# Performance work log

Measured on AMD Instinct MI355X. Metric: run time of the kernel, lower is better.

Reference implementation:

```python
import jax, jax.numpy as jnp
import numpy as np

N = 50000; E = 400000; H = 8; D = 32; CD = 768; SD = 128; OUT = 2; HD = H * D


def gat_conv(x, src, dst, W, a_src, a_dst, b):
    """PyG-style GATConv (concat heads, self-loops, LeakyReLU 0.2, eval mode)."""
    n = x.shape[0]
    loops = jnp.arange(n, dtype=src.dtype)
    s = jnp.concatenate([src, loops])
    t = jnp.concatenate([dst, loops])
    h = (x @ W).reshape(n, H, D)                      # [N,H,D]
    a_s = (h * a_src).sum(-1)                          # [N,H]
    a_d = (h * a_dst).sum(-1)                          # [N,H]
    e = jax.nn.leaky_relu(a_s[s] + a_d[t], 0.2)        # [E+N,H]
    m = jax.ops.segment_max(e, t, num_segments=n)
    m = jnp.where(jnp.isfinite(m), m, 0.0)
    ex = jnp.exp(e - m[t])
    den = jax.ops.segment_sum(ex, t, num_segments=n)
    alpha = ex / (den[t] + 1e-16)                      # segment softmax over incoming edges
    out = jax.ops.segment_sum(alpha[:, :, None] * h[s], t, num_segments=n)
    return out.reshape(n, HD) + b


def setup_inputs():
    key = jax.random.key(0)
    ks = jax.random.split(key, 32)
    inp = {}
    inp['content_x'] = jax.random.normal(ks[0], (N, CD), jnp.float32)
    inp['social_x'] = jax.random.normal(ks[1], (N, SD), jnp.float32)
    inp['content_edge_index'] = jax.random.randint(ks[2], (2, E), 0, N, dtype=jnp.int32)
    inp['social_edge_index'] = jax.random.randint(ks[3], (2, E), 0, N, dtype=jnp.int32)
    i = 4
    def mk(shape, scale=0.05):
        nonlocal i
        w = jax.random.normal(ks[i], shape, jnp.float32) * scale
        i += 1
        return w
    # content GAT layers
    inp['Wc0'] = mk((CD, HD)); inp['ac0s'] = mk((H, D)); inp['ac0d'] = mk((H, D)); inp['bc0'] = jnp.zeros((HD,), jnp.float32)
    inp['Wc1'] = mk((HD, HD)); inp['ac1s'] = mk((H, D)); inp['ac1d'] = mk((H, D)); inp['bc1'] = jnp.zeros((HD,), jnp.float32)
    # social GAT layers
    inp['Ws0'] = mk((SD, HD)); inp['as0s'] = mk((H, D)); inp['as0d'] = mk((H, D)); inp['bs0'] = jnp.zeros((HD,), jnp.float32)
    inp['Ws1'] = mk((HD, HD)); inp['as1s'] = mk((H, D)); inp['as1d'] = mk((H, D)); inp['bs1'] = jnp.zeros((HD,), jnp.float32)
    # dual channel attention (Linear(HD,1) each)
    inp['attc_w'] = mk((HD, 1)); inp['attc_b'] = jnp.zeros((1,), jnp.float32)
    inp['atts_w'] = mk((HD, 1)); inp['atts_b'] = jnp.zeros((1,), jnp.float32)
    # MLP head
    inp['fc1_w'] = mk((2 * HD, D)); inp['fc1_b'] = jnp.zeros((D,), jnp.float32)
    inp['fc2_w'] = mk((D, OUT)); inp['fc2_b'] = jnp.zeros((OUT,), jnp.float32)
    return inp


def reference(content_x, social_x, content_edge_index, social_edge_index,
              Wc0, ac0s, ac0d, bc0, Wc1, ac1s, ac1d, bc1,
              Ws0, as0s, as0d, bs0, Ws1, as1s, as1d, bs1,
              attc_w, attc_b, atts_w, atts_b,
              fc1_w, fc1_b, fc2_w, fc2_b):
    cs, cd = content_edge_index[0], content_edge_index[1]
    ss, sd = social_edge_index[0], social_edge_index[1]
    c = jax.nn.elu(gat_conv(content_x, cs, cd, Wc0, ac0s, ac0d, bc0))
    c = jax.nn.elu(gat_conv(c, cs, cd, Wc1, ac1s, ac1d, bc1))
    s = jax.nn.elu(gat_conv(social_x, ss, sd, Ws0, as0s, as0d, bs0))
    s = jax.nn.elu(gat_conv(s, ss, sd, Ws1, as1s, as1d, bs1))
    c_score = jax.nn.sigmoid(c @ attc_w + attc_b)      # [N,1]
    s_score = jax.nn.sigmoid(s @ atts_w + atts_b)      # [N,1]
    w = jax.nn.softmax(jnp.concatenate([c_score, s_score], axis=1), axis=1)  # [N,2]
    x = jnp.concatenate([c * w[:, 0:1], s * w[:, 1:2]], axis=1)
    x = jax.nn.elu(x @ fc1_w + fc1_b)
    x = x @ fc2_w + fc2_b
    return jax.nn.log_softmax(x, axis=1)
```

## Files before the change

### kernel.cpp

```cpp
#include <hip/hip_runtime.h>
#include <cstddef>

#define HD 256
#define NHEAD 8
#define DHEAD 32
#define CAP 64

__global__ __launch_bounds__(256) void zero32_k(int* __restrict__ p, int n) {
    int i = blockIdx.x * 256 + threadIdx.x;
    if (i < n) p[i] = 0;
}

__global__ __launch_bounds__(256) void bucket_fill_k(const int* __restrict__ src,
                                                     const int* __restrict__ dst,
                                                     int* __restrict__ cnt,
                                                     int* __restrict__ bkt, int E) {
    int e = blockIdx.x * 256 + threadIdx.x;
    if (e >= E) return;
    int t = dst[e];
    int pos = atomicAdd(&cnt[t], 1);
    if (pos < CAP) bkt[(size_t)t * CAP + pos] = src[e];
}

__global__ __launch_bounds__(256) void gemm256_k(const float* __restrict__ A,
                                                 const float* __restrict__ B,
                                                 float* __restrict__ C, int M, int K) {
    __shared__ float As[8][132];
    __shared__ float Bs[8][132];
    const int tid = threadIdx.x;
    const int bm = blockIdx.y * 128;
    const int bn = blockIdx.x * 128;
    const int ty = tid >> 4, tx = tid & 15;

    const int arow = tid >> 1, akc = (tid & 1) * 4;
    int grow = bm + arow; if (grow > M - 1) grow = M - 1;
    const float* aptr = A + (size_t)grow * K + akc;

    const int bkr = tid >> 5, bcol = (tid & 31) * 4;
    const float* bptr = B + (size_t)bkr * HD + bn + bcol;

    float acc[8][8];
#pragma unroll
    for (int i = 0; i < 8; i++)
#pragma unroll
        for (int j = 0; j < 8; j++) acc[i][j] = 0.f;

    for (int k0 = 0; k0 < K; k0 += 8) {
        float4 av = *(const float4*)aptr; aptr += 8;
        float4 bv = *(const float4*)bptr; bptr += 8 * HD;
        __syncthreads();
        As[akc + 0][arow] = av.x;
        As[akc + 1][arow] = av.y;
        As[akc + 2][arow] = av.z;
        As[akc + 3][arow] = av.w;
        *(float4*)&Bs[bkr][bcol] = bv;
        __syncthreads();
#pragma unroll
        for (int kk = 0; kk < 8; kk++) {
            float af[8], bf[8];
            *(float4*)(af)     = *(const float4*)&As[kk][ty * 8];
            *(float4*)(af + 4) = *(const float4*)&As[kk][ty * 8 + 4];
            *(float4*)(bf)     = *(const float4*)&Bs[kk][tx * 8];
            *(float4*)(bf + 4) = *(const float4*)&Bs[kk][tx * 8 + 4];
#pragma unroll
            for (int i = 0; i < 8; i++)
#pragma unroll
                for (int j = 0; j < 8; j++)
                    acc[i][j] = fmaf(af[i], bf[j], acc[i][j]);
        }
    }
#pragma unroll
    for (int i = 0; i < 8; i++) {
        int r = bm + ty * 8 + i;
        if (r < M) {
            float* cp = C + (size_t)r * HD + bn + tx * 8;
            *(float4*)cp       = make_float4(acc[i][0], acc[i][1], acc[i][2], acc[i][3]);
            *(float4*)(cp + 4) = make_float4(acc[i][4], acc[i][5], acc[i][6], acc[i][7]);
        }
    }
}

__global__ __launch_bounds__(256) void attscore_k(const float* __restrict__ h,
                                                  const float* __restrict__ a_src,
                                                  const float* __restrict__ a_dst,
                                                  float* __restrict__ out_s,
                                                  float* __restrict__ out_d, int n) {
    int idx = blockIdx.x * 256 + threadIdx.x;
    if (idx >= n * NHEAD) return;
    int head = idx & 7;
    const float* hp = h + (size_t)(idx >> 3) * HD + head * DHEAD;
    const float* ap = a_src + head * DHEAD;
    const float* dp = a_dst + head * DHEAD;
    float s = 0.f, d = 0.f;
#pragma unroll
    for (int j = 0; j < DHEAD; j += 4) {
        float4 hv = *(const float4*)(hp + j);
        float4 av = *(const float4*)(ap + j);
        float4 dv = *(const float4*)(dp + j);
        s += hv.x * av.x + hv.y * av.y + hv.z * av.z + hv.w * av.w;
        d += hv.x * dv.x + hv.y * dv.y + hv.z * dv.z + hv.w * dv.w;
    }
    out_s[idx] = s;
    out_d[idx] = d;
}

__device__ __forceinline__ float leaky02(float x) { return x > 0.f ? x : 0.2f * x; }

__global__ __launch_bounds__(256) void agg_k(const float* __restrict__ h,
                                             const float* __restrict__ a_s,
                                             const float* __restrict__ a_d,
                                             const int* __restrict__ cnt,
                                             const int* __restrict__ bkt,
                                             const float* __restrict__ bias,
                                             float* __restrict__ out, int n) {
    int wid = (blockIdx.x * 256 + threadIdx.x) >> 6;
    if (wid >= n) return;
    int lane = threadIdx.x & 63;
    int head = lane >> 3;
    const float4* h4 = (const float4*)h;

    float adt = a_d[wid * NHEAD + head];
    float m = leaky02(a_s[wid * NHEAD + head] + adt);
    float den = 1.f;
    float4 hv = h4[(size_t)wid * 64 + lane];
    float ax = hv.x, ay = hv.y, az = hv.z, aw = hv.w;

    int k = cnt[wid]; if (k > CAP) k = CAP;
    const int* bp = bkt + (size_t)wid * CAP;
    for (int i = 0; i < k; i++) {
        int s = bp[i];
        float e = leaky02(a_s[s * NHEAD + head] + adt);
        float nm = fmaxf(m, e);
        float corr = __expf(m - nm);
        float p = __expf(e - nm);
        float4 v = h4[(size_t)s * 64 + lane];
        den = den * corr + p;
        ax = ax * corr + p * v.x;
        ay = ay * corr + p * v.y;
        az = az * corr + p * v.z;
        aw = aw * corr + p * v.w;
        m = nm;
    }
    float inv = 1.f / den;
    float4 bv = *(const float4*)(bias + lane * 4);
    float ox = fmaf(ax, inv, bv.x);
    float oy = fmaf(ay, inv, bv.y);
    float oz = fmaf(az, inv, bv.z);
    float ow = fmaf(aw, inv, bv.w);
    ox = ox > 0.f ? ox : expm1f(ox);
    oy = oy > 0.f ? oy : expm1f(oy);
    oz = oz > 0.f ? oz : expm1f(oz);
    ow = ow > 0.f ? ow : expm1f(ow);
    ((float4*)out)[(size_t)wid * 64 + lane] = make_float4(ox, oy, oz, ow);
}

__global__ __launch_bounds__(256) void head_k(const float* __restrict__ cb,
                                              const float* __restrict__ sb,
                                              const float* __restrict__ attc_w,
                                              const float* __restrict__ attc_b,
                                              const float* __restrict__ atts_w,
                                              const float* __restrict__ atts_b,
                                              const float* __restrict__ fc1_w,
                                              const float* __restrict__ fc1_b,
                                              const float* __restrict__ fc2_w,
                                              const float* __restrict__ fc2_b,
                                              float* __restrict__ out, int n) {
    int wid = (blockIdx.x * 256 + threadIdx.x) >> 6;
    if (wid >= n) return;
    int lane = threadIdx.x & 63;
    const float* c = cb + (size_t)wid * HD;
    const float* s = sb + (size_t)wid * HD;

    float4 cv = *(const float4*)(c + lane * 4);
    float4 wc = *(const float4*)(attc_w + lane * 4);
    float4 sv = *(const float4*)(s + lane * 4);
    float4 ws = *(const float4*)(atts_w + lane * 4);
    float pc = cv.x * wc.x + cv.y * wc.y + cv.z * wc.z + cv.w * wc.w;
    float ps = sv.x * ws.x + sv.y * ws.y + sv.z * ws.z + sv.w * ws.w;
#pragma unroll
    for (int o = 32; o; o >>= 1) { pc += __shfl_xor(pc, o); ps += __shfl_xor(ps, o); }
    float csc = 1.f / (1.f + __expf(-(pc + attc_b[0])));
    float ssc = 1.f / (1.f + __expf(-(ps + atts_b[0])));
    float mx0 = fmaxf(csc, ssc);
    float e0 = __expf(csc - mx0), e1 = __expf(ssc - mx0);
    float w0 = e0 / (e0 + e1), w1 = e1 / (e0 + e1);

    int col = lane & 31, half = lane >> 5;
    const float* xb = half ? s : c;
    float wsc = half ? w1 : w0;
    const float* fw = fc1_w + (size_t)half * HD * 32 + col;
    float acc = 0.f;
#pragma unroll 4
    for (int kk = 0; kk < HD; kk++) acc = fmaf(xb[kk], fw[kk * 32], acc);
    acc *= wsc;
    float y = acc + __shfl_xor(acc, 32) + fc1_b[col];
    y = y > 0.f ? y : expm1f(y);
    float v = y * fc2_w[col * 2 + half];
#pragma unroll
    for (int o = 16; o; o >>= 1) v += __shfl_xor(v, o);
    float z0 = __shfl(v, 0), z1 = __shfl(v, 32);
    if (lane == 0) {
        float zm = fmaxf(z0, z1);
        float lse = zm + log1pf(__expf(fminf(z0, z1) - zm));
        out[(size_t)wid * 2]     = z0 - lse;
        out[(size_t)wid * 2 + 1] = z1 - lse;
    }
}

extern "C" void kernel_launch(void* const* d_in, const int* in_sizes, int n_in,
                              void* d_out, int out_size, void* d_ws, size_t ws_size,
                              hipStream_t stream) {
    (void)n_in; (void)out_size; (void)ws_size;
    const float* content_x = (const float*)d_in[0];
    const float* social_x  = (const float*)d_in[1];
    const int*   cei = (const int*)d_in[2];
    const int*   sei = (const int*)d_in[3];
    const float* Wc0  = (const float*)d_in[4];
    const float* ac0s = (const float*)d_in[5];
    const float* ac0d = (const float*)d_in[6];
    const float* bc0  = (const float*)d_in[7];
    const float* Wc1  = (const float*)d_in[8];
    const float* ac1s = (const float*)d_in[9];
    const float* ac1d = (const float*)d_in[10];
    const float* bc1  = (const float*)d_in[11];
    const float* Ws0  = (const float*)d_in[12];
    const float* as0s = (const float*)d_in[13];
    const float* as0d = (const float*)d_in[14];
    const float* bs0  = (const float*)d_in[15];
    const float* Ws1  = (const float*)d_in[16];
    const float* as1s = (const float*)d_in[17];
    const float* as1d = (const float*)d_in[18];
    const float* bs1  = (const float*)d_in[19];
    const float* attc_w = (const float*)d_in[20];
    const float* attc_b = (const float*)d_in[21];
    const float* atts_w = (const float*)d_in[22];
    const float* atts_b = (const float*)d_in[23];
    const float* fc1_w  = (const float*)d_in[24];
    const float* fc1_b  = (const float*)d_in[25];
    const float* fc2_w  = (const float*)d_in[26];
    const float* fc2_b  = (const float*)d_in[27];

    const int E  = in_sizes[2] / 2;
    const int CD = in_sizes[4] / HD;
    const int SD = in_sizes[12] / HD;
    const int n  = in_sizes[0] / CD;

    char* p = (char*)d_ws;
    auto carve = [&](size_t bytes) { char* q = p; p += (bytes + 255) & ~(size_t)255; return q; };
    float* hbuf = (float*)carve((size_t)n * HD * 4);
    float* cbuf = (float*)carve((size_t)n * HD * 4);
    float* sbuf = (float*)carve((size_t)n * HD * 4);
    float* asb  = (float*)carve((size_t)n * NHEAD * 4);
    float* adb  = (float*)carve((size_t)n * NHEAD * 4);
    int* cnt_c  = (int*)carve((size_t)n * 4);
    int* cnt_s  = (int*)carve((size_t)n * 4);
    int* bkt_c  = (int*)carve((size_t)n * CAP * 4);
    int* bkt_s  = (int*)carve((size_t)n * CAP * 4);

    zero32_k<<<dim3((n + 255) / 256), 256, 0, stream>>>(cnt_c, n);
    zero32_k<<<dim3((n + 255) / 256), 256, 0, stream>>>(cnt_s, n);
    bucket_fill_k<<<dim3((E + 255) / 256), 256, 0, stream>>>(cei, cei + E, cnt_c, bkt_c, E);
    bucket_fill_k<<<dim3((E + 255) / 256), 256, 0, stream>>>(sei, sei + E, cnt_s, bkt_s, E);

    dim3 gg(2, (n + 127) / 128);
    dim3 nb8((n * NHEAD + 255) / 256);
    dim3 nwave((n + 3) / 4);

    gemm256_k<<<gg, 256, 0, stream>>>(content_x, Wc0, hbuf, n, CD);
    attscore_k<<<nb8, 256, 0, stream>>>(hbuf, ac0s, ac0d, asb, adb, n);
    agg_k<<<nwave, 256, 0, stream>>>(hbuf, asb, adb, cnt_c, bkt_c, bc0, cbuf, n);
    gemm256_k<<<gg, 256, 0, stream>>>(cbuf, Wc1, hbuf, n, HD);
    attscore_k<<<nb8, 256, 0, stream>>>(hbuf, ac1s, ac1d, asb, adb, n);
    agg_k<<<nwave, 256, 0, stream>>>(hbuf, asb, adb, cnt_c, bkt_c, bc1, cbuf, n);
    gemm256_k<<<gg, 256, 0, stream>>>(social_x, Ws0, hbuf, n, SD);
    attscore_k<<<nb8, 256, 0, stream>>>(hbuf, as0s, as0d, asb, adb, n);
    agg_k<<<nwave, 256, 0, stream>>>(hbuf, asb, adb, cnt_s, bkt_s, bs0, sbuf, n);
    gemm256_k<<<gg, 256, 0, stream>>>(sbuf, Ws1, hbuf, n, HD);
    attscore_k<<<nb8, 256, 0, stream>>>(hbuf, as1s, as1d, asb, adb, n);
    agg_k<<<nwave, 256, 0, stream>>>(hbuf, asb, adb, cnt_s, bkt_s, bs1, sbuf, n);

    head_k<<<nwave, 256, 0, stream>>>(cbuf, sbuf, attc_w, attc_b, atts_w, atts_b,
                                      fc1_w, fc1_b, fc2_w, fc2_b, (float*)d_out, n);
}
```

Baseline: 1.397 ms.

## Replace FP32 SIMT GEMM with split-bf16 MFMA GEMM using direct-to-LDS loads

Replaces the scalar FP32 GEMM with a matrix-core kernel that emulates FP32 through a three-term bf16 hi/lo split (hi*hi + hi*lo + lo*hi). Inputs and weights are pre-split into bf16 hi/lo buffers. The layer-0 aggregation kernel writes its output already split, which feeds the layer-1 GEMM. Tiles are staged through swizzled LDS with global_load_lds. The intent is to move the dominant GEMM cost (especially the 768-wide content projection) onto MFMA units. The cost is extra split passes, added memory traffic, and a small loss of accuracy from dropping the lo*lo term.

```diff
diff --git a/kernel.cpp b/kernel.cpp
--- a/kernel.cpp
+++ b/kernel.cpp
@@ -1,10 +1,28 @@
 #include <hip/hip_runtime.h>
 #include <cstddef>
+#include <cstdint>
 
 #define HD 256
 #define NHEAD 8
-#define DHEAD 32
 #define CAP 64
+
+typedef __attribute__((ext_vector_type(8))) short bf16x8;
+typedef __attribute__((ext_vector_type(4))) float f32x4;
+
+__device__ __forceinline__ unsigned short f2bf(float f) {
+    unsigned u = __float_as_uint(f);
+    u += 0x7fffu + ((u >> 16) & 1u);
+    return (unsigned short)(u >> 16);
+}
+__device__ __forceinline__ float bf2f(unsigned short h) {
+    return __uint_as_float(((unsigned)h) << 16);
+}
+
+__device__ __forceinline__ void gload16(const unsigned short* g, unsigned short* l) {
+    __builtin_amdgcn_global_load_lds((const __attribute__((address_space(1))) unsigned int*)g,
+                                     (__attribute__((address_space(3))) unsigned int*)l,
+                                     16, 0, 0);
+}
 
 __global__ __launch_bounds__(256) void zero32_k(int* __restrict__ p, int n) {
     int i = blockIdx.x * 256 + threadIdx.x;
@@ -22,60 +40,123 @@
     if (pos < CAP) bkt[(size_t)t * CAP + pos] = src[e];
 }
 
-__global__ __launch_bounds__(256) void gemm256_k(const float* __restrict__ A,
-                                                 const float* __restrict__ B,
-                                                 float* __restrict__ C, int M, int K) {
-    __shared__ float As[8][132];
-    __shared__ float Bs[8][132];
+__global__ __launch_bounds__(256) void split_k(const float* __restrict__ x,
+                                               unsigned short* __restrict__ hi,
+                                               unsigned short* __restrict__ lo,
+                                               int n4) {
+    int i = blockIdx.x * 256 + threadIdx.x;
+    int stride = gridDim.x * 256;
+    for (; i < n4; i += stride) {
+        float4 v = ((const float4*)x)[i];
+        ushort4 h, l;
+        h.x = f2bf(v.x); l.x = f2bf(v.x - bf2f(h.x));
+        h.y = f2bf(v.y); l.y = f2bf(v.y - bf2f(h.y));
+        h.z = f2bf(v.z); l.z = f2bf(v.z - bf2f(h.z));
+        h.w = f2bf(v.w); l.w = f2bf(v.w - bf2f(h.w));
+        ((ushort4*)hi)[i] = h;
+        ((ushort4*)lo)[i] = l;
+    }
+}
+
+__global__ __launch_bounds__(256) void wsplit_k(const float* __restrict__ W,
+                                                unsigned short* __restrict__ hi,
+                                                unsigned short* __restrict__ lo, int K) {
+    int idx = blockIdx.x * 256 + threadIdx.x;
+    if (idx >= K * HD) return;
+    int n = idx / K, k = idx - n * K;
+    float v = W[(size_t)k * HD + n];
+    unsigned short h = f2bf(v);
+    hi[idx] = h;
+    lo[idx] = f2bf(v - bf2f(h));
+}
+
+__global__ __launch_bounds__(256, 2) void gemm_mfma_k(
+    const unsigned short* __restrict__ Ahi, const unsigned short* __restrict__ Alo,
+    const unsigned short* __restrict__ Bhi, const unsigned short* __restrict__ Blo,
+    float* __restrict__ C, int M, int K) {
+    __shared__ unsigned short smem[4 * 128 * 32];
     const int tid = threadIdx.x;
+    const int lane = tid & 63;
+    const int wv = tid >> 6;
+    const int Rw = (wv >> 1) * 64;
+    const int Cw = (wv & 1) * 64;
     const int bm = blockIdx.y * 128;
     const int bn = blockIdx.x * 128;
-    const int ty = tid >> 4, tx = tid & 15;
-
-    const int arow = tid >> 1, akc = (tid & 1) * 4;
-    int grow = bm + arow; if (grow > M - 1) grow = M - 1;
-    const float* aptr = A + (size_t)grow * K + akc;
-
-    const int bkr = tid >> 5, bcol = (tid & 31) * 4;
-    const float* bptr = B + (size_t)bkr * HD + bn + bcol;
-
-    float acc[8][8];
-#pragma unroll
-    for (int i = 0; i < 8; i++)
-#pragma unroll
-        for (int j = 0; j < 8; j++) acc[i][j] = 0.f;
-
-    for (int k0 = 0; k0 < K; k0 += 8) {
-        float4 av = *(const float4*)aptr; aptr += 8;
-        float4 bv = *(const float4*)bptr; bptr += 8 * HD;
+
+    const int sr0 = tid >> 2;
+    const int p = tid & 3;
+    const int g0 = p ^ ((sr0 >> 1) & 3);
+    const int g1 = p ^ (((sr0 + 64) >> 1) & 3);
+    int ar0 = bm + sr0;      if (ar0 >= M) ar0 = M - 1;
+    int ar1 = bm + sr0 + 64; if (ar1 >= M) ar1 = M - 1;
+    const int bc0 = bn + sr0;
+    const int bc1 = bn + sr0 + 64;
+    const size_t aoff0 = (size_t)ar0 * K + g0 * 8;
+    const size_t aoff1 = (size_t)ar1 * K + g1 * 8;
+    const size_t boff0 = (size_t)bc0 * K + g0 * 8;
+    const size_t boff1 = (size_t)bc1 * K + g1 * 8;
+
+    unsigned short* sAh = smem;
+    unsigned short* sAl = smem + 4096;
+    unsigned short* sBh = smem + 8192;
+    unsigned short* sBl = smem + 12288;
+    const int ldsb = wv * 512;
+
+    f32x4 acc[4][4];
+#pragma unroll
+    for (int m = 0; m < 4; m++)
+#pragma unroll
+        for (int n = 0; n < 4; n++) acc[m][n] = (f32x4){0.f, 0.f, 0.f, 0.f};
+
+    const int r16 = lane & 15, gq = lane >> 4;
+    const int rsw = gq ^ ((r16 >> 1) & 3);
+
+    for (int k0 = 0; k0 < K; k0 += 32) {
         __syncthreads();
-        As[akc + 0][arow] = av.x;
-        As[akc + 1][arow] = av.y;
-        As[akc + 2][arow] = av.z;
-        As[akc + 3][arow] = av.w;
-        *(float4*)&Bs[bkr][bcol] = bv;
+        gload16(Ahi + aoff0 + k0, sAh + ldsb);
+        gload16(Ahi + aoff1 + k0, sAh + 2048 + ldsb);
+        gload16(Alo + aoff0 + k0, sAl + ldsb);
+        gload16(Alo + aoff1 + k0, sAl + 2048 + ldsb);
+        gload16(Bhi + boff0 + k0, sBh + ldsb);
+        gload16(Bhi + boff1 + k0, sBh + 2048 + ldsb);
+        gload16(Blo + boff0 + k0, sBl + ldsb);
+        gload16(Blo + boff1 + k0, sBl + 2048 + ldsb);
         __syncthreads();
-#pragma unroll
-        for (int kk = 0; kk < 8; kk++) {
-            float af[8], bf[8];
-            *(float4*)(af)     = *(const float4*)&As[kk][ty * 8];
-            *(float4*)(af + 4) = *(const float4*)&As[kk][ty * 8 + 4];
-            *(float4*)(bf)     = *(const float4*)&Bs[kk][tx * 8];
-            *(float4*)(bf + 4) = *(const float4*)&Bs[kk][tx * 8 + 4];
-#pragma unroll
-            for (int i = 0; i < 8; i++)
-#pragma unroll
-                for (int j = 0; j < 8; j++)
-                    acc[i][j] = fmaf(af[i], bf[j], acc[i][j]);
+
+        bf16x8 ah[4], al[4], bh[4], bl[4];
+#pragma unroll
+        for (int m = 0; m < 4; m++) {
+            int off = (Rw + m * 16 + r16) * 32 + rsw * 8;
+            ah[m] = *(const bf16x8*)(sAh + off);
+            al[m] = *(const bf16x8*)(sAl + off);
         }
-    }
-#pragma unroll
-    for (int i = 0; i < 8; i++) {
-        int r = bm + ty * 8 + i;
-        if (r < M) {
-            float* cp = C + (size_t)r * HD + bn + tx * 8;
-            *(float4*)cp       = make_float4(acc[i][0], acc[i][1], acc[i][2], acc[i][3]);
-            *(float4*)(cp + 4) = make_float4(acc[i][4], acc[i][5], acc[i][6], acc[i][7]);
+#pragma unroll
+        for (int n = 0; n < 4; n++) {
+            int off = (Cw + n * 16 + r16) * 32 + rsw * 8;
+            bh[n] = *(const bf16x8*)(sBh + off);
+            bl[n] = *(const bf16x8*)(sBl + off);
+        }
+#pragma unroll
+        for (int m = 0; m < 4; m++)
+#pragma unroll
+            for (int n = 0; n < 4; n++) {
+                acc[m][n] = __builtin_amdgcn_mfma_f32_16x16x32_bf16(ah[m], bh[n], acc[m][n], 0, 0, 0);
+                acc[m][n] = __builtin_amdgcn_mfma_f32_16x16x32_bf16(ah[m], bl[n], acc[m][n], 0, 0, 0);
+                acc[m][n] = __builtin_amdgcn_mfma_f32_16x16x32_bf16(al[m], bh[n], acc[m][n], 0, 0, 0);
+            }
+    }
+
+#pragma unroll
+    for (int m = 0; m < 4; m++) {
+        int rbase = bm + Rw + m * 16 + ((lane >> 4) << 2);
+#pragma unroll
+        for (int n = 0; n < 4; n++) {
+            int col = bn + Cw + n * 16 + r16;
+            float* cp = C + (size_t)rbase * HD + col;
+            f32x4 v = acc[m][n];
+#pragma unroll
+            for (int r = 0; r < 4; r++)
+                if (rbase + r < M) cp[(size_t)r * HD] = v[r];
         }
     }
 }
@@ -88,12 +169,12 @@
     int idx = blockIdx.x * 256 + threadIdx.x;
     if (idx >= n * NHEAD) return;
     int head = idx & 7;
-    const float* hp = h + (size_t)(idx >> 3) * HD + head * DHEAD;
-    const float* ap = a_src + head * DHEAD;
-    const float* dp = a_dst + head * DHEAD;
+    const float* hp = h + (size_t)(idx >> 3) * HD + head * 32;
+    const float* ap = a_src + head * 32;
+    const float* dp = a_dst + head * 32;
     float s = 0.f, d = 0.f;
 #pragma unroll
-    for (int j = 0; j < DHEAD; j += 4) {
+    for (int j = 0; j < 32; j += 4) {
         float4 hv = *(const float4*)(hp + j);
         float4 av = *(const float4*)(ap + j);
         float4 dv = *(const float4*)(dp + j);
@@ -112,7 +193,9 @@
                                              const int* __restrict__ cnt,
                                              const int* __restrict__ bkt,
                                              const float* __restrict__ bias,
-                                             float* __restrict__ out, int n) {
+                                             float* __restrict__ out,
+                                             unsigned short* __restrict__ ohi,
+                                             unsigned short* __restrict__ olo, int n) {
     int wid = (blockIdx.x * 256 + threadIdx.x) >> 6;
     if (wid >= n) return;
     int lane = threadIdx.x & 63;
@@ -132,13 +215,13 @@
         float e = leaky02(a_s[s * NHEAD + head] + adt);
         float nm = fmaxf(m, e);
         float corr = __expf(m - nm);
-        float p = __expf(e - nm);
+        float pp = __expf(e - nm);
         float4 v = h4[(size_t)s * 64 + lane];
-        den = den * corr + p;
-        ax = ax * corr + p * v.x;
-        ay = ay * corr + p * v.y;
-        az = az * corr + p * v.z;
-        aw = aw * corr + p * v.w;
+        den = den * corr + pp;
+        ax = ax * corr + pp * v.x;
+        ay = ay * corr + pp * v.y;
+        az = az * corr + pp * v.z;
+        aw = aw * corr + pp * v.w;
         m = nm;
     }
     float inv = 1.f / den;
@@ -152,6 +235,15 @@
     oz = oz > 0.f ? oz : expm1f(oz);
     ow = ow > 0.f ? ow : expm1f(ow);
     ((float4*)out)[(size_t)wid * 64 + lane] = make_float4(ox, oy, oz, ow);
+    if (ohi) {
+        ushort4 h4o, l4o;
+        h4o.x = f2bf(ox); l4o.x = f2bf(ox - bf2f(h4o.x));
+        h4o.y = f2bf(oy); l4o.y = f2bf(oy - bf2f(h4o.y));
+        h4o.z = f2bf(oz); l4o.z = f2bf(oz - bf2f(h4o.z));
+        h4o.w = f2bf(ow); l4o.w = f2bf(ow - bf2f(h4o.w));
+        ((ushort4*)ohi)[(size_t)wid * 64 + lane] = h4o;
+        ((ushort4*)olo)[(size_t)wid * 64 + lane] = l4o;
+    }
 }
 
 __global__ __launch_bounds__(256) void head_k(const float* __restrict__ cb,
@@ -250,35 +342,55 @@
     float* hbuf = (float*)carve((size_t)n * HD * 4);
     float* cbuf = (float*)carve((size_t)n * HD * 4);
     float* sbuf = (float*)carve((size_t)n * HD * 4);
+    unsigned short* Xhi = (unsigned short*)carve((size_t)n * CD * 2);
+    unsigned short* Xlo = (unsigned short*)carve((size_t)n * CD * 2);
     float* asb  = (float*)carve((size_t)n * NHEAD * 4);
     float* adb  = (float*)carve((size_t)n * NHEAD * 4);
     int* cnt_c  = (int*)carve((size_t)n * 4);
     int* cnt_s  = (int*)carve((size_t)n * 4);
     int* bkt_c  = (int*)carve((size_t)n * CAP * 4);
     int* bkt_s  = (int*)carve((size_t)n * CAP * 4);
-
-    zero32_k<<<dim3((n + 255) / 256), 256, 0, stream>>>(cnt_c, n);
-    zero32_k<<<dim3((n + 255) / 256), 256, 0, stream>>>(cnt_s, n);
-    bucket_fill_k<<<dim3((E + 255) / 256), 256, 0, stream>>>(cei, cei + E, cnt_c, bkt_c, E);
-    bucket_fill_k<<<dim3((E + 255) / 256), 256, 0, stream>>>(sei, sei + E, cnt_s, bkt_s, E);
+    unsigned short* Wc0h = (unsigned short*)carve((size_t)CD * HD * 2);
+    unsigned short* Wc0l = (unsigned short*)carve((size_t)CD * HD * 2);
+    unsigned short* Wc1h = (unsigned short*)carve((size_t)HD * HD * 2);
+    unsigned short* Wc1l = (unsigned short*)carve((size_t)HD * HD * 2);
+    unsigned short* Ws0h = (unsigned short*)carve((size_t)SD * HD * 2);
+    unsigned short* Ws0l = (unsigned short*)carve((size_t)SD * HD * 2);
+    unsigned short* Ws1h = (unsigned short*)carve((size_t)HD * HD * 2);
+    unsigned short* Ws1l = (unsigned short*)carve((size_t)HD * HD * 2);
+
+    dim3 b256(256);
+    zero32_k<<<dim3((n + 255) / 256), b256, 0, stream>>>(cnt_c, n);
+    zero32_k<<<dim3((n + 255) / 256), b256, 0, stream>>>(cnt_s, n);
+    bucket_fill_k<<<dim3((E + 255) / 256), b256, 0, stream>>>(cei, cei + E, cnt_c, bkt_c, E);
+    bucket_fill_k<<<dim3((E + 255) / 256), b256, 0, stream>>>(sei, sei + E, cnt_s, bkt_s, E);
+
+    wsplit_k<<<dim3((CD * HD + 255) / 256), b256, 0, stream>>>(Wc0, Wc0h, Wc0l, CD);
+    wsplit_k<<<dim3((HD * HD + 255) / 256), b256, 0, stream>>>(Wc1, Wc1h, Wc1l, HD);
+    wsplit_k<<<dim3((SD * HD + 255) / 256), b256, 0, stream>>>(Ws0, Ws0h, Ws0l, SD);
+    wsplit_k<<<dim3((HD * HD + 255) / 256), b256, 0, stream>>>(Ws1, Ws1h, Ws1l, HD);
 
     dim3 gg(2, (n + 127) / 128);
     dim3 nb8((n * NHEAD + 255) / 256);
     dim3 nwave((n + 3) / 4);
 
-    gemm256_k<<<gg, 256, 0, stream>>>(content_x, Wc0, hbuf, n, CD);
-    attscore_k<<<nb8, 256, 0, stream>>>(hbuf, ac0s, ac0d, asb, adb, n);
-    agg_k<<<nwave, 256, 0, stream>>>(hbuf, asb, adb, cnt_c, bkt_c, bc0, cbuf, n);
-    gemm256_k<<<gg, 256, 0, stream>>>(cbuf, Wc1, hbuf, n, HD);
-    attscore_k<<<nb8, 256, 0, stream>>>(hbuf, ac1s, ac1d, asb, adb, n);
-    agg_k<<<nwave, 256, 0, stream>>>(hbuf, asb, adb, cnt_c, bkt_c, bc1, cbuf, n);
-    gemm256_k<<<gg, 256, 0, stream>>>(social_x, Ws0, hbuf, n, SD);
-    attscore_k<<<nb8, 256, 0, stream>>>(hbuf, as0s, as0d, asb, adb, n);
-    agg_k<<<nwave, 256, 0, stream>>>(hbuf, asb, adb, cnt_s, bkt_s, bs0, sbuf, n);
-    gemm256_k<<<gg, 256, 0, stream>>>(sbuf, Ws1, hbuf, n, HD);
-    attscore_k<<<nb8, 256, 0, stream>>>(hbuf, as1s, as1d, asb, adb, n);
-    agg_k<<<nwave, 256, 0, stream>>>(hbuf, asb, adb, cnt_s, bkt_s, bs1, sbuf, n);
-
-    head_k<<<nwave, 256, 0, stream>>>(cbuf, sbuf, attc_w, attc_b, atts_w, atts_b,
-                                      fc1_w, fc1_b, fc2_w, fc2_b, (float*)d_out, n);
-}
+    split_k<<<dim3(2048), b256, 0, stream>>>(content_x, Xhi, Xlo, n * CD / 4);
+    gemm_mfma_k<<<gg, b256, 0, stream>>>(Xhi, Xlo, Wc0h, Wc0l, hbuf, n, CD);
+    attscore_k<<<nb8, b256, 0, stream>>>(hbuf, ac0s, ac0d, asb, adb, n);
+    agg_k<<<nwave, b256, 0, stream>>>(hbuf, asb, adb, cnt_c, bkt_c, bc0, cbuf, Xhi, Xlo, n);
+    gemm_mfma_k<<<gg, b256, 0, stream>>>(Xhi, Xlo, Wc1h, Wc1l, hbuf, n, HD);
+    attscore_k<<<nb8, b256, 0, stream>>>(hbuf, ac1s, ac1d, asb, adb, n);
+    agg_k<<<nwave, b256, 0, stream>>>(hbuf, asb, adb, cnt_c, bkt_c, bc1, cbuf,
+                                      (unsigned short*)nullptr, (unsigned short*)nullptr, n);
+    split_k<<<dim3(2048), b256, 0, stream>>>(social_x, Xhi, Xlo, n * SD / 4);
+    gemm_mfma_k<<<gg, b256, 0, stream>>>(Xhi, Xlo, Ws0h, Ws0l, hbuf, n, SD);
+    attscore_k<<<nb8, b256, 0, stream>>>(hbuf, as0s, as0d, asb, adb, n);
+    agg_k<<<nwave, b256, 0, stream>>>(hbuf, asb, adb, cnt_s, bkt_s, bs0, sbuf, Xhi, Xlo, n);
+    gemm_mfma_k<<<gg, b256, 0, stream>>>(Xhi, Xlo, Ws1h, Ws1l, hbuf, n, HD);
+    attscore_k<<<nb8, b256, 0, stream>>>(hbuf, as1s, as1d, asb, adb, n);
+    agg_k<<<nwave, b256, 0, stream>>>(hbuf, asb, adb, cnt_s, bkt_s, bs1, sbuf,
+                                      (unsigned short*)nullptr, (unsigned short*)nullptr, n);
+
+    head_k<<<nwave, b256, 0, stream>>>(cbuf, sbuf, attc_w, attc_b, atts_w, atts_b,
+                                       fc1_w, fc1_b, fc2_w, fc2_b, (float*)d_out, n);
+}
```

Result: faster. 1.152 ms (-17.5%).
